# Kernel optimization log

Measured on AMD Instinct MI355X. Metric: run time of the kernel, lower is better.

The kernel has to match this reference:

```python
import jax, jax.numpy as jnp
import numpy as np

D_MODEL = 2048
N_HEADS = 16
D_HEAD = 128
INIT_RANGE = 0.02
EPSILON = -100000.0  # mask fill value from the original module


def setup_inputs() -> dict:
    key = jax.random.key(0)
    ks = jax.random.split(key, 6)
    x = jax.random.normal(ks[0], (2, 2048, D_MODEL), dtype=jnp.float32)
    W_Q = jax.random.normal(ks[1], (N_HEADS, D_MODEL, D_HEAD), dtype=jnp.float32) * INIT_RANGE
    W_K = jax.random.normal(ks[2], (N_HEADS, D_MODEL, D_HEAD), dtype=jnp.float32) * INIT_RANGE
    W_V = jax.random.normal(ks[3], (N_HEADS, D_MODEL, D_HEAD), dtype=jnp.float32) * INIT_RANGE
    W_O = jax.random.normal(ks[4], (N_HEADS, D_HEAD, D_MODEL), dtype=jnp.float32) * INIT_RANGE
    b_Q = jnp.zeros((N_HEADS, D_HEAD), dtype=jnp.float32)
    b_K = jnp.zeros((N_HEADS, D_HEAD), dtype=jnp.float32)
    b_V = jnp.zeros((N_HEADS, D_HEAD), dtype=jnp.float32)
    b_O = jnp.zeros((D_MODEL,), dtype=jnp.float32)
    return {"normalized_resid_pre": x, "W_Q": W_Q, "b_Q": b_Q, "W_K": W_K,
            "b_K": b_K, "W_V": W_V, "b_V": b_V, "W_O": W_O, "b_O": b_O}


def reference(normalized_resid_pre, W_Q, b_Q, W_K, b_K, W_V, b_V, W_O, b_O):
    x = normalized_resid_pre  # [b, s, d_model]
    # per-head projections: [b, s, h, d_head]
    q = jnp.einsum('bsd,hdk->bshk', x, W_Q) + b_Q
    k = jnp.einsum('bsd,hdk->bshk', x, W_K) + b_K
    v = jnp.einsum('bsd,hdk->bshk', x, W_V) + b_V
    # attention scores [b, h, q, k]
    scores = jnp.einsum('bqhk,bshk->bhqs', q, k) / jnp.sqrt(jnp.float32(D_HEAD))
    S = scores.shape[-1]
    causal = jnp.tril(jnp.ones((S, S), dtype=bool))  # True = keep
    scores = jnp.where(causal, scores, jnp.float32(EPSILON))
    pattern = jax.nn.softmax(scores, axis=-1)
    z = jnp.einsum('bhqs,bshk->bqhk', pattern, v)
    attn_out = jnp.einsum('bqhk,hkd->bqd', z, W_O) + b_O
    return attn_out
```

## Files before the change

### kernel.cpp

```cpp
#include <hip/hip_runtime.h>
#include <hip/hip_bf16.h>

typedef unsigned short bfu;
typedef short          bf16x8 __attribute__((ext_vector_type(8)));
typedef float          floatx4 __attribute__((ext_vector_type(4)));
typedef unsigned short bfu4 __attribute__((ext_vector_type(4)));

__device__ __forceinline__ bfu f2bf(float f) {
    __hip_bfloat16 h = __float2bfloat16(f);
    return __builtin_bit_cast(unsigned short, h);
}

__device__ __forceinline__ void glds16(const bfu* g, bfu* l) {
    __builtin_amdgcn_global_load_lds(
        (const __attribute__((address_space(1))) unsigned int*)g,
        (__attribute__((address_space(3))) unsigned int*)l, 16, 0, 0);
}

#define BATCH 2
#define SEQ   2048
#define DM    2048
#define NH    16
#define DKH   128
#define SCALE 0.08838834764831845f

__global__ __launch_bounds__(256)
void cvt_x(const float* __restrict__ x, bfu* __restrict__ xb, int n) {
    const int i = (blockIdx.x * 256 + threadIdx.x) * 4;
    if (i >= n) return;
    const float4 v = *(const float4*)(x + i);
    bfu4 p; p[0] = f2bf(v.x); p[1] = f2bf(v.y); p[2] = f2bf(v.z); p[3] = f2bf(v.w);
    *(bfu4*)(xb + i) = p;
}

__global__ __launch_bounds__(256)
void tcvt(const float* __restrict__ in, bfu* __restrict__ out, int R, int C, float s) {
    __shared__ float tile[32][33];
    const int bz = blockIdx.z;
    const float* src = in + (size_t)bz * R * C;
    bfu* dst = out + (size_t)bz * R * C;
    const int c0 = blockIdx.x * 32, r0 = blockIdx.y * 32;
    const int tx = threadIdx.x, ty = threadIdx.y;
    #pragma unroll
    for (int i = 0; i < 4; i++)
        tile[ty + i*8][tx] = src[(size_t)(r0 + ty + i*8) * C + c0 + tx];
    __syncthreads();
    #pragma unroll
    for (int i = 0; i < 4; i++)
        dst[(size_t)(c0 + ty + i*8) * R + r0 + tx] = f2bf(tile[tx][ty + i*8] * s);
}

__global__ __launch_bounds__(256)
void proj_gemm(const bfu* __restrict__ xb, const bfu* __restrict__ Wt,
               const float* __restrict__ bias, float bscale,
               bfu* Out, bfu* Vt, int vmode) {
    __shared__ bfu As[128 * 32];
    __shared__ bfu Bs[128 * 32];
    const int tid  = threadIdx.x;
    const int lane = tid & 63;
    const int wave = tid >> 6;
    const int lrow = lane & 15;
    const int quad = lane >> 4;
    const int mw = (wave & 1) * 64;
    const int nw = (wave >> 1) * 64;
    const size_t m0 = (size_t)blockIdx.x * 128;
    const size_t n0 = (size_t)blockIdx.y * 128;
    const int rowb = lane >> 2;
    const int colb = (lane & 3) * 8;

    floatx4 acc[4][4] = {};

    for (int k0 = 0; k0 < DM; k0 += 32) {
        __syncthreads();
        #pragma unroll
        for (int i = 0; i < 2; i++) {
            const int rg = wave * 2 + i;
            glds16(xb + (m0 + rg*16 + rowb) * DM + k0 + colb, &As[rg * 512]);
            glds16(Wt + (n0 + rg*16 + rowb) * DM + k0 + colb, &Bs[rg * 512]);
        }
        __syncthreads();
        bf16x8 af[4], bfr[4];
        #pragma unroll
        for (int t = 0; t < 4; t++) {
            af[t]  = *(const bf16x8*)&As[(mw + t*16 + lrow) * 32 + quad * 8];
            bfr[t] = *(const bf16x8*)&Bs[(nw + t*16 + lrow) * 32 + quad * 8];
        }
        #pragma unroll
        for (int mt = 0; mt < 4; mt++)
            #pragma unroll
            for (int nt = 0; nt < 4; nt++)
                acc[mt][nt] = __builtin_amdgcn_mfma_f32_16x16x32_bf16(
                                  af[mt], bfr[nt], acc[mt][nt], 0, 0, 0);
    }

    if (vmode == 0) {
        #pragma unroll
        for (int mt = 0; mt < 4; mt++) {
            #pragma unroll
            for (int nt = 0; nt < 4; nt++) {
                const int nl = (int)n0 + nw + nt*16 + lrow;
                const float bv = bias[nl] * bscale;
                #pragma unroll
                for (int r = 0; r < 4; r++) {
                    const size_t gm = m0 + mw + mt*16 + quad*4 + r;
                    Out[gm * DM + nl] = f2bf(acc[mt][nt][r] + bv);
                }
            }
        }
    } else {
        #pragma unroll
        for (int mt = 0; mt < 4; mt++) {
            #pragma unroll
            for (int nt = 0; nt < 4; nt++) {
                const int nl = (int)n0 + nw + nt*16 + lrow;
                const float bv = bias[nl] * bscale;
                const size_t gm0 = m0 + mw + mt*16 + quad*4;
                const int b = (int)(gm0 >> 11), s = (int)(gm0 & 2047);
                bfu4 pk;
                #pragma unroll
                for (int r = 0; r < 4; r++) pk[r] = f2bf(acc[mt][nt][r] + bv);
                *(bfu4*)&Vt[((size_t)(b * NH + (nl >> 7)) * DKH + (nl & 127)) * SEQ + s] = pk;
            }
        }
    }
}

__global__ __launch_bounds__(256)
void flash_attn(const bfu* __restrict__ Q, const bfu* __restrict__ K,
                const bfu* __restrict__ Vt, bfu* __restrict__ Z) {
    __shared__ bfu Ks[4][64][32];
    __shared__ bfu Vs[2][128][32];
    __shared__ bfu Ps[4][16][80];

    const int tid  = threadIdx.x;
    const int lane = tid & 63;
    const int wave = tid >> 6;
    const int lrow = lane & 15;
    const int quad = lane >> 4;
    const int hb = blockIdx.x;
    const int h = hb & 15, b = hb >> 4;
    const int qt = 31 - blockIdx.y;
    const int q0w = qt * 64 + wave * 16;
    const int rowb = lane >> 2, colb = (lane & 3) * 8;

    const bfu* Qrow = Q + (size_t)(b * SEQ + q0w + lrow) * DM + h * DKH;
    bf16x8 qf[4];
    #pragma unroll
    for (int kc = 0; kc < 4; kc++)
        qf[kc] = *(const bf16x8*)(Qrow + kc*32 + quad*8);

    floatx4 z[8] = {};
    float l_r[4] = {0.f, 0.f, 0.f, 0.f};

    const bfu* Kb = K + (size_t)b * SEQ * DM + h * DKH;
    const bfu* Vb = Vt + (size_t)(b * NH + h) * DKH * SEQ;
    const int ntiles = qt + 1;

    for (int it = 0; it < ntiles; it++) {
        const int s0 = it * 64;
        __syncthreads();
        #pragma unroll
        for (int i = 0; i < 8; i++) {
            const int chunk = wave * 8 + i;
            if (chunk < 16) {
                const int kc = chunk >> 2, kg = chunk & 3;
                glds16(Kb + (size_t)(s0 + kg*16 + rowb) * DM + kc*32 + colb,
                       &Ks[kc][kg*16][0]);
            } else {
                const int c2 = chunk - 16;
                const int sh = c2 >> 3, dg = c2 & 7;
                glds16(Vb + (size_t)(dg*16 + rowb) * SEQ + s0 + sh*32 + colb,
                       &Vs[sh][dg*16][0]);
            }
        }
        __syncthreads();

        floatx4 sc[4];
        #pragma unroll
        for (int st = 0; st < 4; st++) {
            floatx4 a = {};
            #pragma unroll
            for (int kc = 0; kc < 4; kc++) {
                bf16x8 kf = *(const bf16x8*)&Ks[kc][st*16 + lrow][quad*8];
                a = __builtin_amdgcn_mfma_f32_16x16x32_bf16(qf[kc], kf, a, 0, 0, 0);
            }
            sc[st] = a;
        }

        #pragma unroll
        for (int r = 0; r < 4; r++) {
            const int qg = q0w + quad*4 + r;
            float ls = 0.f;
            #pragma unroll
            for (int st = 0; st < 4; st++) {
                const int sg = s0 + st*16 + lrow;
                const float p = (sg <= qg) ? __expf(sc[st][r]) : 0.f;
                sc[st][r] = p;
                ls += p;
                Ps[wave][quad*4 + r][st*16 + lrow] = f2bf(p);
            }
            l_r[r] += ls;
        }

        bf16x8 pf0 = *(const bf16x8*)&Ps[wave][lrow][quad*8];
        bf16x8 pf1 = *(const bf16x8*)&Ps[wave][lrow][32 + quad*8];
        #pragma unroll
        for (int dt = 0; dt < 8; dt++) {
            bf16x8 v0 = *(const bf16x8*)&Vs[0][dt*16 + lrow][quad*8];
            z[dt] = __builtin_amdgcn_mfma_f32_16x16x32_bf16(pf0, v0, z[dt], 0, 0, 0);
            bf16x8 v1 = *(const bf16x8*)&Vs[1][dt*16 + lrow][quad*8];
            z[dt] = __builtin_amdgcn_mfma_f32_16x16x32_bf16(pf1, v1, z[dt], 0, 0, 0);
        }
    }

    float inv[4];
    #pragma unroll
    for (int r = 0; r < 4; r++) {
        float l = l_r[r];
        l += __shfl_xor(l, 1);
        l += __shfl_xor(l, 2);
        l += __shfl_xor(l, 4);
        l += __shfl_xor(l, 8);
        inv[r] = 1.0f / l;
    }
    #pragma unroll
    for (int dt = 0; dt < 8; dt++) {
        #pragma unroll
        for (int r = 0; r < 4; r++) {
            const int qg = q0w + quad*4 + r;
            const int dk = dt*16 + lrow;
            Z[(size_t)(b * SEQ + qg) * DM + h * DKH + dk] = f2bf(z[dt][r] * inv[r]);
        }
    }
}

__global__ __launch_bounds__(256)
void out_gemm(const bfu* __restrict__ Zb, const bfu* __restrict__ WtO,
              const float* __restrict__ bO, float* out) {
    __shared__ bfu As[128 * 32];
    __shared__ bfu Bs[128 * 32];
    const int tid  = threadIdx.x;
    const int lane = tid & 63;
    const int wave = tid >> 6;
    const int lrow = lane & 15;
    const int quad = lane >> 4;
    const int mw = (wave & 1) * 64;
    const int nw = (wave >> 1) * 64;
    const size_t m0 = (size_t)blockIdx.x * 128;
    const size_t n0 = (size_t)blockIdx.y * 128;
    const int rowb = lane >> 2, colb = (lane & 3) * 8;

    floatx4 acc[4][4] = {};

    for (int k0 = 0; k0 < DM; k0 += 32) {
        __syncthreads();
        #pragma unroll
        for (int i = 0; i < 2; i++) {
            const int rg = wave * 2 + i;
            glds16(Zb  + (m0 + rg*16 + rowb) * DM + k0 + colb, &As[rg * 512]);
            glds16(WtO + (n0 + rg*16 + rowb) * DM + k0 + colb, &Bs[rg * 512]);
        }
        __syncthreads();
        bf16x8 af[4], bfr[4];
        #pragma unroll
        for (int t = 0; t < 4; t++) {
            af[t]  = *(const bf16x8*)&As[(mw + t*16 + lrow) * 32 + quad * 8];
            bfr[t] = *(const bf16x8*)&Bs[(nw + t*16 + lrow) * 32 + quad * 8];
        }
        #pragma unroll
        for (int mt = 0; mt < 4; mt++)
            #pragma unroll
            for (int nt = 0; nt < 4; nt++)
                acc[mt][nt] = __builtin_amdgcn_mfma_f32_16x16x32_bf16(
                                  af[mt], bfr[nt], acc[mt][nt], 0, 0, 0);
    }

    #pragma unroll
    for (int mt = 0; mt < 4; mt++) {
        #pragma unroll
        for (int nt = 0; nt < 4; nt++) {
            const size_t gn = n0 + nw + nt*16 + lrow;
            const float bv = bO[gn];
            #pragma unroll
            for (int r = 0; r < 4; r++) {
                const size_t gm = m0 + mw + mt*16 + quad*4 + r;
                out[gm * DM + gn] = acc[mt][nt][r] + bv;
            }
        }
    }
}

extern "C" void kernel_launch(void* const* d_in, const int* in_sizes, int n_in,
                              void* d_out, int out_size, void* d_ws, size_t ws_size,
                              hipStream_t stream) {
    const float* x  = (const float*)d_in[0];
    const float* WQ = (const float*)d_in[1];
    const float* bQ = (const float*)d_in[2];
    const float* WK = (const float*)d_in[3];
    const float* bK = (const float*)d_in[4];
    const float* WV = (const float*)d_in[5];
    const float* bV = (const float*)d_in[6];
    const float* WO = (const float*)d_in[7];
    const float* bO = (const float*)d_in[8];
    float* out = (float*)d_out;
    bfu* ws  = (bfu*)d_ws;
    bfu* dob = (bfu*)d_out;

    bfu* Qall = ws;
    bfu* Kall = Qall + 8388608;
    bfu* Vt   = Kall + 8388608;
    bfu* Zb   = Vt   + 8388608;
    bfu* xb   = dob;
    bfu* Wt   = dob + 8388608;

    const dim3 tb(32, 8, 1);

    cvt_x<<<8192, 256, 0, stream>>>(x, xb, BATCH * SEQ * DM);

    tcvt<<<dim3(4, 64, 16), tb, 0, stream>>>(WQ, Wt, DM, DKH, SCALE);
    proj_gemm<<<dim3(32, 16), 256, 0, stream>>>(xb, Wt, bQ, SCALE, Qall, nullptr, 0);
    tcvt<<<dim3(4, 64, 16), tb, 0, stream>>>(WK, Wt, DM, DKH, 1.0f);
    proj_gemm<<<dim3(32, 16), 256, 0, stream>>>(xb, Wt, bK, 1.0f, Kall, nullptr, 0);
    tcvt<<<dim3(4, 64, 16), tb, 0, stream>>>(WV, Wt, DM, DKH, 1.0f);
    proj_gemm<<<dim3(32, 16), 256, 0, stream>>>(xb, Wt, bV, 1.0f, nullptr, Vt, 1);

    flash_attn<<<dim3(32, 32), 256, 0, stream>>>(Qall, Kall, Vt, Zb);

    tcvt<<<dim3(64, 64, 1), tb, 0, stream>>>(WO, Qall, DM, DM, 1.0f);
    out_gemm<<<dim3(32, 16), 256, 0, stream>>>(Zb, Qall, bO, out);
}
```

Baseline: 405.3 us.

## Batch QKV weight conversion and projections into single launches; transpose score MFMA

```diff
diff --git a/kernel.cpp b/kernel.cpp
--- a/kernel.cpp
+++ b/kernel.cpp
@@ -5,6 +5,7 @@
 typedef short          bf16x8 __attribute__((ext_vector_type(8)));
 typedef float          floatx4 __attribute__((ext_vector_type(4)));
 typedef unsigned short bfu4 __attribute__((ext_vector_type(4)));
+typedef unsigned int   u32x2 __attribute__((ext_vector_type(2)));
 
 __device__ __forceinline__ bfu f2bf(float f) {
     __hip_bfloat16 h = __float2bfloat16(f);
@@ -51,11 +52,42 @@
 }
 
 __global__ __launch_bounds__(256)
-void proj_gemm(const bfu* __restrict__ xb, const bfu* __restrict__ Wt,
-               const float* __restrict__ bias, float bscale,
-               bfu* Out, bfu* Vt, int vmode) {
+void tcvt_qkv(const float* __restrict__ WQ, const float* __restrict__ WK,
+              const float* __restrict__ WV,
+              bfu* __restrict__ WtQ, bfu* __restrict__ WtK, bfu* __restrict__ WtV) {
+    __shared__ float tile[32][33];
+    const int p  = blockIdx.z >> 4;
+    const int bz = blockIdx.z & 15;
+    const float* src = (p == 0) ? WQ : (p == 1) ? WK : WV;
+    bfu*         dst = (p == 0) ? WtQ : (p == 1) ? WtK : WtV;
+    const float  s   = (p == 0) ? SCALE : 1.0f;
+    src += (size_t)bz * DM * DKH;
+    dst += (size_t)bz * DM * DKH;
+    const int c0 = blockIdx.x * 32, r0 = blockIdx.y * 32;
+    const int tx = threadIdx.x, ty = threadIdx.y;
+    #pragma unroll
+    for (int i = 0; i < 4; i++)
+        tile[ty + i*8][tx] = src[(size_t)(r0 + ty + i*8) * DKH + c0 + tx];
+    __syncthreads();
+    #pragma unroll
+    for (int i = 0; i < 4; i++)
+        dst[(size_t)(c0 + ty + i*8) * DM + r0 + tx] = f2bf(tile[tx][ty + i*8] * s);
+}
+
+__global__ __launch_bounds__(256)
+void proj_qkv(const bfu* __restrict__ xb,
+              const bfu* __restrict__ WtQ, const bfu* __restrict__ WtK,
+              const bfu* __restrict__ WtV,
+              const float* __restrict__ bQ, const float* __restrict__ bK,
+              const float* __restrict__ bV,
+              bfu* __restrict__ Qall, bfu* __restrict__ Kall, bfu* __restrict__ Vt) {
     __shared__ bfu As[128 * 32];
     __shared__ bfu Bs[128 * 32];
+    const int p = blockIdx.y >> 4;
+    const bfu*   Wt   = (p == 0) ? WtQ : (p == 1) ? WtK : WtV;
+    const float* bias = (p == 0) ? bQ  : (p == 1) ? bK  : bV;
+    const float bscale = (p == 0) ? SCALE : 1.0f;
+
     const int tid  = threadIdx.x;
     const int lane = tid & 63;
     const int wave = tid >> 6;
@@ -64,7 +96,7 @@
     const int mw = (wave & 1) * 64;
     const int nw = (wave >> 1) * 64;
     const size_t m0 = (size_t)blockIdx.x * 128;
-    const size_t n0 = (size_t)blockIdx.y * 128;
+    const size_t n0 = (size_t)(blockIdx.y & 15) * 128;
     const int rowb = lane >> 2;
     const int colb = (lane & 3) * 8;
 
@@ -93,7 +125,8 @@
                                   af[mt], bfr[nt], acc[mt][nt], 0, 0, 0);
     }
 
-    if (vmode == 0) {
+    if (p < 2) {
+        bfu* Out = (p == 0) ? Qall : Kall;
         #pragma unroll
         for (int mt = 0; mt < 4; mt++) {
             #pragma unroll
@@ -130,7 +163,7 @@
                 const bfu* __restrict__ Vt, bfu* __restrict__ Z) {
     __shared__ bfu Ks[4][64][32];
     __shared__ bfu Vs[2][128][32];
-    __shared__ bfu Ps[4][16][80];
+    __shared__ bfu Ps[4][16][72];
 
     const int tid  = threadIdx.x;
     const int lane = tid & 63;
@@ -150,7 +183,8 @@
         qf[kc] = *(const bf16x8*)(Qrow + kc*32 + quad*8);
 
     floatx4 z[8] = {};
-    float l_r[4] = {0.f, 0.f, 0.f, 0.f};
+    float l_loc = 0.f;
+    const int qg = q0w + lrow;
 
     const bfu* Kb = K + (size_t)b * SEQ * DM + h * DKH;
     const bfu* Vb = Vt + (size_t)(b * NH + h) * DKH * SEQ;
@@ -182,24 +216,23 @@
             #pragma unroll
             for (int kc = 0; kc < 4; kc++) {
                 bf16x8 kf = *(const bf16x8*)&Ks[kc][st*16 + lrow][quad*8];
-                a = __builtin_amdgcn_mfma_f32_16x16x32_bf16(qf[kc], kf, a, 0, 0, 0);
+                a = __builtin_amdgcn_mfma_f32_16x16x32_bf16(kf, qf[kc], a, 0, 0, 0);
             }
             sc[st] = a;
         }
 
         #pragma unroll
-        for (int r = 0; r < 4; r++) {
-            const int qg = q0w + quad*4 + r;
-            float ls = 0.f;
-            #pragma unroll
-            for (int st = 0; st < 4; st++) {
-                const int sg = s0 + st*16 + lrow;
-                const float p = (sg <= qg) ? __expf(sc[st][r]) : 0.f;
-                sc[st][r] = p;
-                ls += p;
-                Ps[wave][quad*4 + r][st*16 + lrow] = f2bf(p);
-            }
-            l_r[r] += ls;
+        for (int st = 0; st < 4; st++) {
+            const int sbase = s0 + st*16 + quad*4;
+            const float p0 = (sbase + 0 <= qg) ? __expf(sc[st][0]) : 0.f;
+            const float p1 = (sbase + 1 <= qg) ? __expf(sc[st][1]) : 0.f;
+            const float p2 = (sbase + 2 <= qg) ? __expf(sc[st][2]) : 0.f;
+            const float p3 = (sbase + 3 <= qg) ? __expf(sc[st][3]) : 0.f;
+            l_loc += (p0 + p1) + (p2 + p3);
+            u32x2 pk;
+            pk[0] = (unsigned)f2bf(p0) | ((unsigned)f2bf(p1) << 16);
+            pk[1] = (unsigned)f2bf(p2) | ((unsigned)f2bf(p3) << 16);
+            *(u32x2*)&Ps[wave][lrow][st*16 + quad*4] = pk;
         }
 
         bf16x8 pf0 = *(const bf16x8*)&Ps[wave][lrow][quad*8];
@@ -213,23 +246,20 @@
         }
     }
 
+    float L = l_loc;
+    L += __shfl_xor(L, 16);
+    L += __shfl_xor(L, 32);
     float inv[4];
     #pragma unroll
-    for (int r = 0; r < 4; r++) {
-        float l = l_r[r];
-        l += __shfl_xor(l, 1);
-        l += __shfl_xor(l, 2);
-        l += __shfl_xor(l, 4);
-        l += __shfl_xor(l, 8);
-        inv[r] = 1.0f / l;
-    }
+    for (int r = 0; r < 4; r++)
+        inv[r] = 1.0f / __shfl(L, quad*4 + r, 64);
     #pragma unroll
     for (int dt = 0; dt < 8; dt++) {
         #pragma unroll
         for (int r = 0; r < 4; r++) {
-            const int qg = q0w + quad*4 + r;
+            const int qq = q0w + quad*4 + r;
             const int dk = dt*16 + lrow;
-            Z[(size_t)(b * SEQ + qg) * DM + h * DKH + dk] = f2bf(z[dt][r] * inv[r]);
+            Z[(size_t)(b * SEQ + qq) * DM + h * DKH + dk] = f2bf(z[dt][r] * inv[r]);
         }
     }
 }
@@ -310,19 +340,18 @@
     bfu* Kall = Qall + 8388608;
     bfu* Vt   = Kall + 8388608;
     bfu* Zb   = Vt   + 8388608;
+    bfu* WtV  = Zb;
     bfu* xb   = dob;
-    bfu* Wt   = dob + 8388608;
+    bfu* WtQ  = dob + 8388608;
+    bfu* WtK  = dob + 12582912;
 
     const dim3 tb(32, 8, 1);
 
     cvt_x<<<8192, 256, 0, stream>>>(x, xb, BATCH * SEQ * DM);
 
-    tcvt<<<dim3(4, 64, 16), tb, 0, stream>>>(WQ, Wt, DM, DKH, SCALE);
-    proj_gemm<<<dim3(32, 16), 256, 0, stream>>>(xb, Wt, bQ, SCALE, Qall, nullptr, 0);
-    tcvt<<<dim3(4, 64, 16), tb, 0, stream>>>(WK, Wt, DM, DKH, 1.0f);
-    proj_gemm<<<dim3(32, 16), 256, 0, stream>>>(xb, Wt, bK, 1.0f, Kall, nullptr, 0);
-    tcvt<<<dim3(4, 64, 16), tb, 0, stream>>>(WV, Wt, DM, DKH, 1.0f);
-    proj_gemm<<<dim3(32, 16), 256, 0, stream>>>(xb, Wt, bV, 1.0f, nullptr, Vt, 1);
+    tcvt_qkv<<<dim3(4, 64, 48), tb, 0, stream>>>(WQ, WK, WV, WtQ, WtK, WtV);
+    proj_qkv<<<dim3(32, 48), 256, 0, stream>>>(xb, WtQ, WtK, WtV,
+                                               bQ, bK, bV, Qall, Kall, Vt);
 
     flash_attn<<<dim3(32, 32), 256, 0, stream>>>(Qall, Kall, Vt, Zb);
 
```

Measured after the change: 368.8 us. 9.0% less time.
